# Optimization experiments

Hardware: AMD Instinct MI355X
Metric: run time of the kernel (lower is better)

The kernel has to match this reference:

```python
import jax, jax.numpy as jnp
import numpy as np

VOCAB, E = 100000, 128
B, S = 256, 512

def setup_inputs() -> dict:
    key = jax.random.key(0)
    k1, k2, k3, k4, k5, k6 = jax.random.split(key, 6)
    x = jax.random.randint(k1, (B, S), 0, VOCAB, dtype=jnp.int64 if jax.config.jax_enable_x64 else jnp.int32)
    emb = jax.random.normal(k2, (VOCAB, E), dtype=jnp.float32) * 0.02
    Wq = jax.random.normal(k3, (E, 1), dtype=jnp.float32) * (1.0 / np.sqrt(E))
    bq = jax.random.normal(k4, (1,), dtype=jnp.float32) * 0.01
    Wm = jax.random.normal(k5, (E, 2), dtype=jnp.float32) * (1.0 / np.sqrt(E))
    bm = jax.random.normal(k6, (2,), dtype=jnp.float32) * 0.01
    return {"x": x, "emb": emb, "Wq": Wq, "bq": bq, "Wm": Wm, "bm": bm}

def reference(x, emb, Wq, bq, Wm, bm):
    embed_x = emb[x]                                  # [B,S,E] gather
    q = embed_x @ Wq + bq                             # [B,S,1] query projection
    # torch.einsum('ijk,ijk->ij') broadcasts q's size-1 k dim:
    log_p = q[..., 0] * embed_x.sum(axis=-1)          # [B,S]
    p = jax.nn.softmax(log_p, axis=1)                 # softmax over sequence
    t_hat = jnp.einsum('bs,bse->be', p, embed_x)      # attention-weighted pool [B,E]
    return jax.nn.relu(t_hat @ Wm + bm)               # [B,2]
```

## Files before the change

kernel.cpp:

```cpp
#include <hip/hip_runtime.h>
#include <math.h>

#define EDIM 128
#define BB   256
#define SS   512
#define NWAVE 16
#define BLOCK (NWAVE * 64)

template<int CTRL>
__device__ __forceinline__ float dpp_add(float v) {
    int r = __builtin_amdgcn_update_dpp(0, __float_as_int(v), CTRL, 0xF, 0xF, true);
    return v + __int_as_float(r);
}

__device__ __forceinline__ float rowsum16(float v) {
    v = dpp_add<0xB1>(v);
    v = dpp_add<0x4E>(v);
    v = dpp_add<0x124>(v);
    v = dpp_add<0x128>(v);
    return v;
}

__global__ __launch_bounds__(BLOCK)
void fused_embed_attn_kernel(const int* __restrict__ x,
                             const float* __restrict__ emb,
                             const float* __restrict__ Wq,
                             const float* __restrict__ bq,
                             const float* __restrict__ Wm,
                             const float* __restrict__ bm,
                             float* __restrict__ out)
{
    const int b    = blockIdx.x;
    const int tid  = threadIdx.x;
    const int wave = tid >> 6;
    const int lane = tid & 63;
    const int row  = lane >> 4;
    const int slot = lane & 15;
    const int d0   = slot * 8;

    const float4 wq0 = *reinterpret_cast<const float4*>(Wq + d0);
    const float4 wq1 = *reinterpret_cast<const float4*>(Wq + d0 + 4);
    const float  bq0 = bq[0];

    const int tbase = b * SS + wave * 32 + row * 8;
    const int4 ia = *reinterpret_cast<const int4*>(x + tbase);
    const int4 ib = *reinterpret_cast<const int4*>(x + tbase + 4);
    const int idx[8] = {ia.x, ia.y, ia.z, ia.w, ib.x, ib.y, ib.z, ib.w};

    float m = -INFINITY, Z = 0.f;
    float acc[8] = {0.f, 0.f, 0.f, 0.f, 0.f, 0.f, 0.f, 0.f};

    #pragma unroll
    for (int i = 0; i < 8; ++i) {
        const float* rp = emb + (size_t)idx[i] * EDIM + d0;
        const float4 e0 = *reinterpret_cast<const float4*>(rp);
        const float4 e1 = *reinterpret_cast<const float4*>(rp + 4);

        float q = e0.x * wq0.x + e0.y * wq0.y + e0.z * wq0.z + e0.w * wq0.w
                + e1.x * wq1.x + e1.y * wq1.y + e1.z * wq1.z + e1.w * wq1.w;
        float s = e0.x + e0.y + e0.z + e0.w + e1.x + e1.y + e1.z + e1.w;
        q = rowsum16(q);
        s = rowsum16(s);
        const float lp = (q + bq0) * s;

        const float mn = fmaxf(m, lp);
        const float al = __expf(m - mn);
        const float w  = __expf(lp - mn);
        Z = Z * al + w;
        acc[0] = acc[0] * al + w * e0.x;  acc[1] = acc[1] * al + w * e0.y;
        acc[2] = acc[2] * al + w * e0.z;  acc[3] = acc[3] * al + w * e0.w;
        acc[4] = acc[4] * al + w * e1.x;  acc[5] = acc[5] * al + w * e1.y;
        acc[6] = acc[6] * al + w * e1.z;  acc[7] = acc[7] * al + w * e1.w;
        m = mn;
    }

    float m1 = fmaxf(m, __shfl_xor(m, 16));
    const float M  = fmaxf(m1, __shfl_xor(m1, 32));
    const float sc = __expf(m - M);
    float Zs = Z * sc;
    Zs += __shfl_xor(Zs, 16);
    Zs += __shfl_xor(Zs, 32);
    #pragma unroll
    for (int j = 0; j < 8; ++j) {
        float a = acc[j] * sc;
        a += __shfl_xor(a, 16);
        a += __shfl_xor(a, 32);
        acc[j] = a;
    }

    __shared__ float sm[NWAVE];
    __shared__ float szv[NWAVE];
    __shared__ float sacc[NWAVE][EDIM];

    if (row == 0) {
        *reinterpret_cast<float4*>(&sacc[wave][d0])     = make_float4(acc[0], acc[1], acc[2], acc[3]);
        *reinterpret_cast<float4*>(&sacc[wave][d0 + 4]) = make_float4(acc[4], acc[5], acc[6], acc[7]);
        if (slot == 0) { sm[wave] = M; szv[wave] = Zs; }
    }
    __syncthreads();

    if (tid < 64) {
        float Mb = sm[0];
        #pragma unroll
        for (int w = 1; w < NWAVE; ++w) Mb = fmaxf(Mb, sm[w]);
        float zt = 0.f, tv0 = 0.f, tv1 = 0.f;
        #pragma unroll
        for (int w = 0; w < NWAVE; ++w) {
            const float s2 = __expf(sm[w] - Mb);
            zt += szv[w] * s2;
            const float2 a2 = *reinterpret_cast<const float2*>(&sacc[w][2 * tid]);
            tv0 += a2.x * s2;
            tv1 += a2.y * s2;
        }
        const float t0 = tv0 / zt, t1 = tv1 / zt;
        const float4 wm = *reinterpret_cast<const float4*>(Wm + 4 * tid);
        float c0 = t0 * wm.x + t1 * wm.z;
        float c1 = t0 * wm.y + t1 * wm.w;
        #pragma unroll
        for (int off = 32; off >= 1; off >>= 1) {
            c0 += __shfl_xor(c0, off);
            c1 += __shfl_xor(c1, off);
        }
        if (tid == 0) {
            out[b * 2 + 0] = fmaxf(c0 + bm[0], 0.f);
            out[b * 2 + 1] = fmaxf(c1 + bm[1], 0.f);
        }
    }
}

extern "C" void kernel_launch(void* const* d_in, const int* in_sizes, int n_in,
                              void* d_out, int out_size, void* d_ws, size_t ws_size,
                              hipStream_t stream) {
    const int*   x   = (const int*)  d_in[0];
    const float* emb = (const float*)d_in[1];
    const float* Wq  = (const float*)d_in[2];
    const float* bq  = (const float*)d_in[3];
    const float* Wm  = (const float*)d_in[4];
    const float* bm  = (const float*)d_in[5];
    float* out = (float*)d_out;

    hipLaunchKernelGGL(fused_embed_attn_kernel, dim3(BB), dim3(BLOCK), 0,
                       stream, x, emb, Wq, bq, Wm, bm, out);
}
```

Before: 97.24 us.

## Split each batch row across two blocks with atomic last-block merge

Each batch row's sequence is now split between two blocks, giving 512 blocks instead of 256 so more of the GPU's compute units stay busy. Each thread handles 4 tokens instead of 8. Every block writes its partial softmax max, normalizer and weighted sum to workspace. A per-row atomic counter lets the last finishing block merge both halves and compute the output. This adds a memset launch, global workspace traffic and fences, and it reduces the number of gathers each thread has in flight.

Result: slower. 227.0 us (+133.4%).

```diff
diff --git a/kernel.cpp b/kernel.cpp
--- a/kernel.cpp
+++ b/kernel.cpp
@@ -6,6 +6,13 @@
 #define SS   512
 #define NWAVE 16
 #define BLOCK (NWAVE * 64)
+#define NPART 2
+#define TPG   4
+
+#define WS_M    0
+#define WS_Z    512
+#define WS_A    1024
+#define WS_FLAG 66560
 
 template<int CTRL>
 __device__ __forceinline__ float dpp_add(float v) {
@@ -22,15 +29,18 @@
 }
 
 __global__ __launch_bounds__(BLOCK)
-void fused_embed_attn_kernel(const int* __restrict__ x,
-                             const float* __restrict__ emb,
-                             const float* __restrict__ Wq,
-                             const float* __restrict__ bq,
-                             const float* __restrict__ Wm,
-                             const float* __restrict__ bm,
-                             float* __restrict__ out)
+void fused_embed_attn_fused(const int* __restrict__ x,
+                            const float* __restrict__ emb,
+                            const float* __restrict__ Wq,
+                            const float* __restrict__ bq,
+                            const float* __restrict__ Wm,
+                            const float* __restrict__ bm,
+                            float* __restrict__ ws,
+                            float* __restrict__ out)
 {
-    const int b    = blockIdx.x;
+    const int part = blockIdx.x;
+    const int b    = part >> 1;
+    const int half = part & 1;
     const int tid  = threadIdx.x;
     const int wave = tid >> 6;
     const int lane = tid & 63;
@@ -42,16 +52,16 @@
     const float4 wq1 = *reinterpret_cast<const float4*>(Wq + d0 + 4);
     const float  bq0 = bq[0];
 
-    const int tbase = b * SS + wave * 32 + row * 8;
-    const int4 ia = *reinterpret_cast<const int4*>(x + tbase);
-    const int4 ib = *reinterpret_cast<const int4*>(x + tbase + 4);
-    const int idx[8] = {ia.x, ia.y, ia.z, ia.w, ib.x, ib.y, ib.z, ib.w};
+    const int g     = wave * 4 + row;
+    const int tbase = b * SS + half * 256 + g * TPG;
+    const int4 iv   = *reinterpret_cast<const int4*>(x + tbase);
+    const int idx[TPG] = {iv.x, iv.y, iv.z, iv.w};
 
     float m = -INFINITY, Z = 0.f;
     float acc[8] = {0.f, 0.f, 0.f, 0.f, 0.f, 0.f, 0.f, 0.f};
 
     #pragma unroll
-    for (int i = 0; i < 8; ++i) {
+    for (int i = 0; i < TPG; ++i) {
         const float* rp = emb + (size_t)idx[i] * EDIM + d0;
         const float4 e0 = *reinterpret_cast<const float4*>(rp);
         const float4 e1 = *reinterpret_cast<const float4*>(rp + 4);
@@ -90,7 +100,7 @@
 
     __shared__ float sm[NWAVE];
     __shared__ float szv[NWAVE];
-    __shared__ float sacc[NWAVE][EDIM];
+    __shared__ float sacc[NWAVE][EDIM + 4];
 
     if (row == 0) {
         *reinterpret_cast<float4*>(&sacc[wave][d0])     = make_float4(acc[0], acc[1], acc[2], acc[3]);
@@ -99,20 +109,46 @@
     }
     __syncthreads();
 
-    if (tid < 64) {
+    if (tid < EDIM) {
         float Mb = sm[0];
         #pragma unroll
         for (int w = 1; w < NWAVE; ++w) Mb = fmaxf(Mb, sm[w]);
-        float zt = 0.f, tv0 = 0.f, tv1 = 0.f;
+        float zt = 0.f, tv = 0.f;
         #pragma unroll
         for (int w = 0; w < NWAVE; ++w) {
             const float s2 = __expf(sm[w] - Mb);
             zt += szv[w] * s2;
-            const float2 a2 = *reinterpret_cast<const float2*>(&sacc[w][2 * tid]);
-            tv0 += a2.x * s2;
-            tv1 += a2.y * s2;
+            tv += sacc[w][tid] * s2;
         }
-        const float t0 = tv0 / zt, t1 = tv1 / zt;
+        ws[WS_A + part * EDIM + tid] = tv;
+        if (tid == 0) { ws[WS_M + part] = Mb; ws[WS_Z + part] = zt; }
+    }
+    __syncthreads();
+
+    __shared__ int s_win;
+    if (tid == 0) {
+        __threadfence();
+        int* flags = reinterpret_cast<int*>(ws) + WS_FLAG;
+        const int old = atomicAdd(&flags[b], 1);
+        s_win = (old == NPART - 1);
+    }
+    __syncthreads();
+    if (!s_win) return;
+    __threadfence();
+
+    if (tid < 64) {
+        const float m0 = ws[WS_M + b * 2],  m1v = ws[WS_M + b * 2 + 1];
+        const float z0 = ws[WS_Z + b * 2],  z1v = ws[WS_Z + b * 2 + 1];
+        const float Mx = fmaxf(m0, m1v);
+        const float s0 = __expf(m0 - Mx);
+        const float s1 = __expf(m1v - Mx);
+        const float zt = z0 * s0 + z1v * s1;
+
+        const float2 a0 = *reinterpret_cast<const float2*>(ws + WS_A + (b * 2)     * EDIM + 2 * tid);
+        const float2 a1 = *reinterpret_cast<const float2*>(ws + WS_A + (b * 2 + 1) * EDIM + 2 * tid);
+        const float t0 = (a0.x * s0 + a1.x * s1) / zt;
+        const float t1 = (a0.y * s0 + a1.y * s1) / zt;
+
         const float4 wm = *reinterpret_cast<const float4*>(Wm + 4 * tid);
         float c0 = t0 * wm.x + t1 * wm.z;
         float c1 = t0 * wm.y + t1 * wm.w;
@@ -138,7 +174,11 @@
     const float* Wm  = (const float*)d_in[4];
     const float* bm  = (const float*)d_in[5];
     float* out = (float*)d_out;
+    float* ws  = (float*)d_ws;
 
-    hipLaunchKernelGGL(fused_embed_attn_kernel, dim3(BB), dim3(BLOCK), 0,
-                       stream, x, emb, Wq, bq, Wm, bm, out);
+    hipMemsetAsync((char*)d_ws + WS_FLAG * sizeof(float), 0,
+                   BB * sizeof(int), stream);
+
+    hipLaunchKernelGGL(fused_embed_attn_fused, dim3(NPART * BB), dim3(BLOCK), 0,
+                       stream, x, emb, Wq, bq, Wm, bm, ws, out);
 }
```
